# Performance work log

Measured on AMD Instinct MI355X. Metric: run time of the kernel, lower is better.

The kernel has to match this reference:

```python
import jax, jax.numpy as jnp
import numpy as np

B, L, H, NUM_LABELS = 4, 256, 768, 13


def setup_inputs() -> dict:
    key = jax.random.key(0)
    k1, k2, k3, k4, k5 = jax.random.split(key, 5)
    s1 = 1.0 / np.sqrt(2 * H)
    s2 = 1.0 / np.sqrt(H)
    return {
        "hidden_states": jax.random.normal(k1, (B, L, H), dtype=jnp.float32),
        "W1": jax.random.uniform(k2, (2 * H, H), jnp.float32, -s1, s1),
        "b1": jax.random.uniform(k3, (H,), jnp.float32, -s1, s1),
        "W2": jax.random.uniform(k4, (H, NUM_LABELS), jnp.float32, -s2, s2),
        "b2": jax.random.uniform(k5, (NUM_LABELS,), jnp.float32, -s2, s2),
    }


def reference(hidden_states, W1, b1, W2, b2):
    # Original: ffn(cat([x_start expand over dim2, x_end expand over dim1], -1))
    # Algebraically: Linear(2H->H) on the concat == proj(x_start) + proj(x_end)
    # broadcast over the L x L span grid, avoiding the (B,L,L,2H) tensor.
    H_ = hidden_states.shape[-1]
    xs_proj = jnp.einsum('bsh,hk->bsk', hidden_states, W1[:H_])   # start half
    xe_proj = jnp.einsum('bsh,hk->bsk', hidden_states, W1[H_:])   # end half
    h = xs_proj[:, :, None, :] + xe_proj[:, None, :, :] + b1      # (B,L,L,H)
    h = jax.nn.gelu(h, approximate=False)                         # torch GELU default = exact erf
    logits = jnp.einsum('bijk,kn->bijn', h, W2) + b2              # (B,L,L,num_labels)
    return logits
```

## Files before the change

### kernel.cpp

```cpp
#include <hip/hip_runtime.h>
#include <math.h>

#define H 768
#define L 256
#define NB 4
#define NL 13

typedef _Float16 h2 __attribute__((ext_vector_type(2)));
typedef _Float16 h4 __attribute__((ext_vector_type(4)));
typedef _Float16 half8 __attribute__((ext_vector_type(8)));
typedef float f32x4 __attribute__((ext_vector_type(4)));

__device__ inline h2 gelu_pk(h2 x) {
    const _Float16 kC = (_Float16)3.75f;
    h2 hi = {kC, kC}, lo = {(_Float16)-3.75f, (_Float16)-3.75f};
    h2 xc = __builtin_elementwise_min(__builtin_elementwise_max(x, lo), hi);
    h2 u = xc * xc;
    const _Float16 kE = (_Float16)0.125f;
    h2 ve = {kE, kE};
    h2 v = u * ve;
    const _Float16 d4v = (_Float16)0.0832840f,  d3v = (_Float16)-0.4335206f;
    const _Float16 d2v = (_Float16)0.8960128f,  d1v = (_Float16)-0.9876456f;
    const _Float16 d0v = (_Float16)0.7946463f;
    h2 d4 = {d4v, d4v}, d3 = {d3v, d3v}, d2 = {d2v, d2v}, d1 = {d1v, d1v}, d0 = {d0v, d0v};
    h2 p = v * (v * (v * (v * d4 + d3) + d2) + d1) + d0;
    h2 t = xc * p;
    const _Float16 kH = (_Float16)0.5f;
    h2 halfv = {kH, kH};
    h2 hx = x * halfv;
    return hx * t + hx;
}

__global__ __launch_bounds__(256) void gemm_fused(
    const float* __restrict__ X, const float* __restrict__ W1,
    const float* __restrict__ b1, const float* __restrict__ W2,
    _Float16* __restrict__ Pxs2, _Float16* __restrict__ Pxe,
    _Float16* __restrict__ Bfrag2)
{
    const int tid = threadIdx.x;

    if (blockIdx.y == 24) {
        int base = blockIdx.x * 768 + tid;
        #pragma unroll
        for (int r = 0; r < 3; ++r) {
            int idx = base + r * 256;
            int u = idx & 7;
            int lane = (idx >> 3) & 63;
            int kb = idx >> 9;
            int k = kb * 32 + ((lane >> 4) << 3) + u;
            int n = lane & 15;
            float v = (n < NL) ? W2[(size_t)k * NL + n] : 0.f;
            Bfrag2[idx] = (_Float16)v;
        }
        return;
    }

    __shared__ _Float16 As[64][72];
    __shared__ _Float16 Bs[64][72];
    const int w = tid >> 6, lane = tid & 63;
    const int ln = lane & 15, quad = lane >> 4;
    const int m0 = blockIdx.x * 64;
    const int n0g = blockIdx.y * 64;
    const bool isE = (n0g >= H);
    const float* Wb = W1 + (isE ? (size_t)H * H : 0);
    const int c0 = isE ? (n0g - H) : n0g;

    const int ar = tid >> 4;
    const int ac = (tid & 15) * 4;
    const int bc = (tid & 15) * 4;

    f32x4 acc[2][2] = {};
    for (int kr = 0; kr < H / 64; ++kr) {
        const int k0 = kr * 64;
        #pragma unroll
        for (int r = 0; r < 4; ++r) {
            int arow = r * 16 + ar;
            float4 f = *(const float4*)&X[(size_t)(m0 + arow) * H + k0 + ac];
            h4 o = { (_Float16)f.x, (_Float16)f.y, (_Float16)f.z, (_Float16)f.w };
            *(h4*)&As[arow][ac] = o;
        }
        #pragma unroll
        for (int r = 0; r < 2; ++r) {
            int kpl = r * 16 + (tid >> 4);
            const float* wr = &Wb[(size_t)(k0 + 2 * kpl) * H + c0 + bc];
            float4 fa = *(const float4*)wr;
            float4 fb = *(const float4*)(wr + H);
            h2 p0 = {(_Float16)fa.x, (_Float16)fb.x};
            h2 p1 = {(_Float16)fa.y, (_Float16)fb.y};
            h2 p2 = {(_Float16)fa.z, (_Float16)fb.z};
            h2 p3 = {(_Float16)fa.w, (_Float16)fb.w};
            *(h2*)&Bs[bc + 0][2 * kpl] = p0;
            *(h2*)&Bs[bc + 1][2 * kpl] = p1;
            *(h2*)&Bs[bc + 2][2 * kpl] = p2;
            *(h2*)&Bs[bc + 3][2 * kpl] = p3;
        }
        __syncthreads();
        #pragma unroll
        for (int sub = 0; sub < 2; ++sub) {
            const int ko = sub * 32 + quad * 8;
            half8 a0 = *(const half8*)&As[(w & 1) * 32 + ln][ko];
            half8 a1 = *(const half8*)&As[(w & 1) * 32 + 16 + ln][ko];
            half8 b0 = *(const half8*)&Bs[(w >> 1) * 32 + ln][ko];
            half8 b1f = *(const half8*)&Bs[(w >> 1) * 32 + 16 + ln][ko];
            acc[0][0] = __builtin_amdgcn_mfma_f32_16x16x32_f16(a0, b0, acc[0][0], 0, 0, 0);
            acc[0][1] = __builtin_amdgcn_mfma_f32_16x16x32_f16(a0, b1f, acc[0][1], 0, 0, 0);
            acc[1][0] = __builtin_amdgcn_mfma_f32_16x16x32_f16(a1, b0, acc[1][0], 0, 0, 0);
            acc[1][1] = __builtin_amdgcn_mfma_f32_16x16x32_f16(a1, b1f, acc[1][1], 0, 0, 0);
        }
        __syncthreads();
    }

    const int mb = m0 + (w & 1) * 32;
    const int nb = (w >> 1) * 32;
    if (!isE) {
        float bv[2] = { b1[n0g + nb + ln], b1[n0g + nb + 16 + ln] };
        #pragma unroll
        for (int mt = 0; mt < 2; ++mt)
            #pragma unroll
            for (int nt = 0; nt < 2; ++nt) {
                int n = n0g + nb + nt * 16 + ln;
                #pragma unroll
                for (int r = 0; r < 4; ++r) {
                    int m = mb + mt * 16 + quad * 4 + r;
                    Pxs2[(size_t)m * H + n] = (_Float16)(acc[mt][nt][r] + bv[nt]);
                }
            }
    } else {
        #pragma unroll
        for (int mt = 0; mt < 2; ++mt)
            #pragma unroll
            for (int nt = 0; nt < 2; ++nt) {
                int n = c0 + nb + nt * 16 + ln;
                #pragma unroll
                for (int r = 0; r < 4; ++r) {
                    int m = mb + mt * 16 + quad * 4 + r;
                    Pxe[(size_t)m * H + n] = (_Float16)acc[mt][nt][r];
                }
            }
    }
}

__global__ __launch_bounds__(256, 4) void span_mfma_kernel(
    const _Float16* __restrict__ Pxs2, const _Float16* __restrict__ Pxe,
    const _Float16* __restrict__ Bfrag2, const float* __restrict__ b2,
    float* __restrict__ out)
{
    __shared__ unsigned int xsf[4 * H / 2];
    const int ip = blockIdx.x >> 2;
    const int jq = blockIdx.x & 3;
    const int bi0 = ip * 4;
    const int b = bi0 >> 8;
    const int tid = threadIdx.x;

    const unsigned int* xsrc = (const unsigned int*)(Pxs2 + (size_t)bi0 * H);
    #pragma unroll
    for (int t = 0; t < 6; ++t) xsf[t * 256 + tid] = xsrc[t * 256 + tid];

    const int wave = tid >> 6;
    const int lane = tid & 63;
    const int n = lane & 15;
    const int quad = lane >> 4;
    const int j_load = jq * 64 + wave * 16 + n;

    const _Float16* xerow = Pxe + (size_t)(b * L + j_load) * H + quad * 8;
    const half8* bptr = (const half8*)(Bfrag2 + (size_t)lane * 8);

    f32x4 acc[4] = {};
    __syncthreads();

    for (int kb = 0; kb < H / 32; ++kb) {
        half8 bfrag = bptr[kb * 64];
        uint4 xev = *(const uint4*)(xerow + kb * 32);
        h2 xep[4] = { __builtin_bit_cast(h2, xev.x), __builtin_bit_cast(h2, xev.y),
                      __builtin_bit_cast(h2, xev.z), __builtin_bit_cast(h2, xev.w) };
        const int xo = kb * 16 + quad * 4;

        #pragma unroll
        for (int i01 = 0; i01 < 4; ++i01) {
            uint4 xsd = *(const uint4*)&xsf[i01 * (H / 2) + xo];
            h2 xsp[4] = { __builtin_bit_cast(h2, xsd.x), __builtin_bit_cast(h2, xsd.y),
                          __builtin_bit_cast(h2, xsd.z), __builtin_bit_cast(h2, xsd.w) };
            unsigned int pk[4];
            #pragma unroll
            for (int p = 0; p < 4; ++p) {
                h2 g = gelu_pk(xsp[p] + xep[p]);
                pk[p] = __builtin_bit_cast(unsigned int, g);
            }
            uint4 pk4 = {pk[0], pk[1], pk[2], pk[3]};
            half8 afrag = __builtin_bit_cast(half8, pk4);
            acc[i01] = __builtin_amdgcn_mfma_f32_16x16x32_f16(afrag, bfrag, acc[i01], 0, 0, 0);
        }
    }

    if (n < NL) {
        float b2v = b2[n];
        #pragma unroll
        for (int i01 = 0; i01 < 4; ++i01)
            #pragma unroll
            for (int r = 0; r < 4; ++r) {
                int j = jq * 64 + wave * 16 + quad * 4 + r;
                out[((size_t)(bi0 + i01) * L + j) * NL + n] = acc[i01][r] + b2v;
            }
    }
}

extern "C" void kernel_launch(void* const* d_in, const int* in_sizes, int n_in,
                              void* d_out, int out_size, void* d_ws, size_t ws_size,
                              hipStream_t stream)
{
    (void)in_sizes; (void)n_in; (void)out_size; (void)ws_size;
    const float* X  = (const float*)d_in[0];
    const float* W1 = (const float*)d_in[1];
    const float* b1 = (const float*)d_in[2];
    const float* W2 = (const float*)d_in[3];
    const float* b2 = (const float*)d_in[4];
    float* out = (float*)d_out;

    char* ws = (char*)d_ws;
    _Float16* Pxs2   = (_Float16*)ws;
    _Float16* Pxe    = Pxs2 + (size_t)NB * L * H;
    _Float16* Bfrag2 = Pxe + (size_t)NB * L * H;

    gemm_fused<<<dim3(16, 25), 256, 0, stream>>>(X, W1, b1, W2, Pxs2, Pxe, Bfrag2);
    span_mfma_kernel<<<NB * L, 256, 0, stream>>>(Pxs2, Pxe, Bfrag2, b2, out);
}
```

Baseline: 123.8 us.

## Merge projection GEMM and span kernel into one persistent ticket-scheduled kernel

Replaces the two launches with a single kernel of 1024 blocks. Blocks first take GEMM tiles through an atomic ticket counter and signal per-tile completion flags. Each block then spin-waits only on the flags for the start and end projection tiles it needs before running its span computation. W2 fragments are now rebuilt in LDS by every block rather than once in global memory. The goal is to remove the kernel boundary and overlap GEMM tail with span work, at the cost of a memset, atomics, spin-waiting, and more LDS per block, which may lower occupancy.

```diff
diff --git a/kernel.cpp b/kernel.cpp
--- a/kernel.cpp
+++ b/kernel.cpp
@@ -5,6 +5,9 @@
 #define L 256
 #define NB 4
 #define NL 13
+#define MT_TILES 16
+#define NT_TILES 24
+#define N_TICKETS (MT_TILES * NT_TILES)
 
 typedef _Float16 h2 __attribute__((ext_vector_type(2)));
 typedef _Float16 h4 __attribute__((ext_vector_type(4)));
@@ -31,145 +34,156 @@
     return hx * t + hx;
 }
 
-__global__ __launch_bounds__(256) void gemm_fused(
+__global__ __launch_bounds__(256, 3) void mono_kernel(
     const float* __restrict__ X, const float* __restrict__ W1,
     const float* __restrict__ b1, const float* __restrict__ W2,
+    const float* __restrict__ b2,
     _Float16* __restrict__ Pxs2, _Float16* __restrict__ Pxe,
-    _Float16* __restrict__ Bfrag2)
+    int* __restrict__ ctrl, float* __restrict__ out)
 {
-    const int tid = threadIdx.x;
-
-    if (blockIdx.y == 24) {
-        int base = blockIdx.x * 768 + tid;
-        #pragma unroll
-        for (int r = 0; r < 3; ++r) {
-            int idx = base + r * 256;
-            int u = idx & 7;
-            int lane = (idx >> 3) & 63;
-            int kb = idx >> 9;
-            int k = kb * 32 + ((lane >> 4) << 3) + u;
-            int n = lane & 15;
-            float v = (n < NL) ? W2[(size_t)k * NL + n] : 0.f;
-            Bfrag2[idx] = (_Float16)v;
-        }
-        return;
-    }
-
     __shared__ _Float16 As[64][72];
     __shared__ _Float16 Bs[64][72];
+    __shared__ _Float16 w2f[24 * 64 * 8];
+    __shared__ unsigned int xsf[4 * H / 2];
+    __shared__ int s_ticket;
+
+    const int tid = threadIdx.x;
     const int w = tid >> 6, lane = tid & 63;
     const int ln = lane & 15, quad = lane >> 4;
-    const int m0 = blockIdx.x * 64;
-    const int n0g = blockIdx.y * 64;
-    const bool isE = (n0g >= H);
-    const float* Wb = W1 + (isE ? (size_t)H * H : 0);
-    const int c0 = isE ? (n0g - H) : n0g;
-
-    const int ar = tid >> 4;
-    const int ac = (tid & 15) * 4;
-    const int bc = (tid & 15) * 4;
-
-    f32x4 acc[2][2] = {};
-    for (int kr = 0; kr < H / 64; ++kr) {
-        const int k0 = kr * 64;
-        #pragma unroll
-        for (int r = 0; r < 4; ++r) {
-            int arow = r * 16 + ar;
-            float4 f = *(const float4*)&X[(size_t)(m0 + arow) * H + k0 + ac];
-            h4 o = { (_Float16)f.x, (_Float16)f.y, (_Float16)f.z, (_Float16)f.w };
-            *(h4*)&As[arow][ac] = o;
+    int* ticket = ctrl;
+    int* flags  = ctrl + 1;
+
+    for (;;) {
+        __syncthreads();
+        if (tid == 0) s_ticket = atomicAdd(ticket, 1);
+        __syncthreads();
+        const int t = s_ticket;
+        if (t >= N_TICKETS) break;
+
+        const int mtile = t / NT_TILES;
+        const int ntile = t % NT_TILES;
+        const int m0 = mtile * 64;
+        const int n0g = ntile * 64;
+        const bool isE = (n0g >= H);
+        const float* Wb = W1 + (isE ? (size_t)H * H : 0);
+        const int c0 = isE ? (n0g - H) : n0g;
+
+        const int ar = tid >> 4;
+        const int ac = (tid & 15) * 4;
+        const int bc = (tid & 15) * 4;
+
+        f32x4 acc[2][2] = {};
+        for (int kr = 0; kr < H / 64; ++kr) {
+            const int k0 = kr * 64;
+            #pragma unroll
+            for (int r = 0; r < 4; ++r) {
+                int arow = r * 16 + ar;
+                float4 f = *(const float4*)&X[(size_t)(m0 + arow) * H + k0 + ac];
+                h4 o = { (_Float16)f.x, (_Float16)f.y, (_Float16)f.z, (_Float16)f.w };
+                *(h4*)&As[arow][ac] = o;
+            }
+            #pragma unroll
+            for (int r = 0; r < 2; ++r) {
+                int kpl = r * 16 + (tid >> 4);
+                const float* wr = &Wb[(size_t)(k0 + 2 * kpl) * H + c0 + bc];
+                float4 fa = *(const float4*)wr;
+                float4 fb = *(const float4*)(wr + H);
+                h2 p0 = {(_Float16)fa.x, (_Float16)fb.x};
+                h2 p1 = {(_Float16)fa.y, (_Float16)fb.y};
+                h2 p2 = {(_Float16)fa.z, (_Float16)fb.z};
+                h2 p3 = {(_Float16)fa.w, (_Float16)fb.w};
+                *(h2*)&Bs[bc + 0][2 * kpl] = p0;
+                *(h2*)&Bs[bc + 1][2 * kpl] = p1;
+                *(h2*)&Bs[bc + 2][2 * kpl] = p2;
+                *(h2*)&Bs[bc + 3][2 * kpl] = p3;
+            }
+            __syncthreads();
+            #pragma unroll
+            for (int sub = 0; sub < 2; ++sub) {
+                const int ko = sub * 32 + quad * 8;
+                half8 a0 = *(const half8*)&As[(w & 1) * 32 + ln][ko];
+                half8 a1 = *(const half8*)&As[(w & 1) * 32 + 16 + ln][ko];
+                half8 b0 = *(const half8*)&Bs[(w >> 1) * 32 + ln][ko];
+                half8 b1f = *(const half8*)&Bs[(w >> 1) * 32 + 16 + ln][ko];
+                acc[0][0] = __builtin_amdgcn_mfma_f32_16x16x32_f16(a0, b0, acc[0][0], 0, 0, 0);
+                acc[0][1] = __builtin_amdgcn_mfma_f32_16x16x32_f16(a0, b1f, acc[0][1], 0, 0, 0);
+                acc[1][0] = __builtin_amdgcn_mfma_f32_16x16x32_f16(a1, b0, acc[1][0], 0, 0, 0);
+                acc[1][1] = __builtin_amdgcn_mfma_f32_16x16x32_f16(a1, b1f, acc[1][1], 0, 0, 0);
+            }
+            __syncthreads();
         }
-        #pragma unroll
-        for (int r = 0; r < 2; ++r) {
-            int kpl = r * 16 + (tid >> 4);
-            const float* wr = &Wb[(size_t)(k0 + 2 * kpl) * H + c0 + bc];
-            float4 fa = *(const float4*)wr;
-            float4 fb = *(const float4*)(wr + H);
-            h2 p0 = {(_Float16)fa.x, (_Float16)fb.x};
-            h2 p1 = {(_Float16)fa.y, (_Float16)fb.y};
-            h2 p2 = {(_Float16)fa.z, (_Float16)fb.z};
-            h2 p3 = {(_Float16)fa.w, (_Float16)fb.w};
-            *(h2*)&Bs[bc + 0][2 * kpl] = p0;
-            *(h2*)&Bs[bc + 1][2 * kpl] = p1;
-            *(h2*)&Bs[bc + 2][2 * kpl] = p2;
-            *(h2*)&Bs[bc + 3][2 * kpl] = p3;
+
+        const int mb = m0 + (w & 1) * 32;
+        const int nb = (w >> 1) * 32;
+        if (!isE) {
+            float bv[2] = { b1[n0g + nb + ln], b1[n0g + nb + 16 + ln] };
+            #pragma unroll
+            for (int mt = 0; mt < 2; ++mt)
+                #pragma unroll
+                for (int nt = 0; nt < 2; ++nt) {
+                    int n = n0g + nb + nt * 16 + ln;
+                    #pragma unroll
+                    for (int r = 0; r < 4; ++r) {
+                        int m = mb + mt * 16 + quad * 4 + r;
+                        Pxs2[(size_t)m * H + n] = (_Float16)(acc[mt][nt][r] + bv[nt]);
+                    }
+                }
+        } else {
+            #pragma unroll
+            for (int mt = 0; mt < 2; ++mt)
+                #pragma unroll
+                for (int nt = 0; nt < 2; ++nt) {
+                    int n = c0 + nb + nt * 16 + ln;
+                    #pragma unroll
+                    for (int r = 0; r < 4; ++r) {
+                        int m = mb + mt * 16 + quad * 4 + r;
+                        Pxe[(size_t)m * H + n] = (_Float16)acc[mt][nt][r];
+                    }
+                }
         }
+        __threadfence();
         __syncthreads();
-        #pragma unroll
-        for (int sub = 0; sub < 2; ++sub) {
-            const int ko = sub * 32 + quad * 8;
-            half8 a0 = *(const half8*)&As[(w & 1) * 32 + ln][ko];
-            half8 a1 = *(const half8*)&As[(w & 1) * 32 + 16 + ln][ko];
-            half8 b0 = *(const half8*)&Bs[(w >> 1) * 32 + ln][ko];
-            half8 b1f = *(const half8*)&Bs[(w >> 1) * 32 + 16 + ln][ko];
-            acc[0][0] = __builtin_amdgcn_mfma_f32_16x16x32_f16(a0, b0, acc[0][0], 0, 0, 0);
-            acc[0][1] = __builtin_amdgcn_mfma_f32_16x16x32_f16(a0, b1f, acc[0][1], 0, 0, 0);
-            acc[1][0] = __builtin_amdgcn_mfma_f32_16x16x32_f16(a1, b0, acc[1][0], 0, 0, 0);
-            acc[1][1] = __builtin_amdgcn_mfma_f32_16x16x32_f16(a1, b1f, acc[1][1], 0, 0, 0);
-        }
-        __syncthreads();
-    }
-
-    const int mb = m0 + (w & 1) * 32;
-    const int nb = (w >> 1) * 32;
-    if (!isE) {
-        float bv[2] = { b1[n0g + nb + ln], b1[n0g + nb + 16 + ln] };
-        #pragma unroll
-        for (int mt = 0; mt < 2; ++mt)
-            #pragma unroll
-            for (int nt = 0; nt < 2; ++nt) {
-                int n = n0g + nb + nt * 16 + ln;
-                #pragma unroll
-                for (int r = 0; r < 4; ++r) {
-                    int m = mb + mt * 16 + quad * 4 + r;
-                    Pxs2[(size_t)m * H + n] = (_Float16)(acc[mt][nt][r] + bv[nt]);
-                }
-            }
-    } else {
-        #pragma unroll
-        for (int mt = 0; mt < 2; ++mt)
-            #pragma unroll
-            for (int nt = 0; nt < 2; ++nt) {
-                int n = c0 + nb + nt * 16 + ln;
-                #pragma unroll
-                for (int r = 0; r < 4; ++r) {
-                    int m = mb + mt * 16 + quad * 4 + r;
-                    Pxe[(size_t)m * H + n] = (_Float16)acc[mt][nt][r];
-                }
-            }
-    }
-}
-
-__global__ __launch_bounds__(256, 4) void span_mfma_kernel(
-    const _Float16* __restrict__ Pxs2, const _Float16* __restrict__ Pxe,
-    const _Float16* __restrict__ Bfrag2, const float* __restrict__ b2,
-    float* __restrict__ out)
-{
-    __shared__ unsigned int xsf[4 * H / 2];
+        if (tid == 0) atomicAdd(&flags[mtile * 2 + (isE ? 1 : 0)], 1);
+    }
+
+    #pragma unroll 4
+    for (int r = 0; r < 48; ++r) {
+        int idx = r * 256 + tid;
+        int u = idx & 7;
+        int l = (idx >> 3) & 63;
+        int kb = idx >> 9;
+        int k = kb * 32 + ((l >> 4) << 3) + u;
+        int n = l & 15;
+        float v = (n < NL) ? W2[(size_t)k * NL + n] : 0.f;
+        w2f[idx] = (_Float16)v;
+    }
+
     const int ip = blockIdx.x >> 2;
     const int jq = blockIdx.x & 3;
     const int bi0 = ip * 4;
     const int b = bi0 >> 8;
-    const int tid = threadIdx.x;
+    const int mt_i = ip >> 4;
+    const int mt_j = b * 4 + jq;
+
+    while (__hip_atomic_load(&flags[mt_i * 2 + 0], __ATOMIC_RELAXED, __HIP_MEMORY_SCOPE_AGENT) < 12 ||
+           __hip_atomic_load(&flags[mt_j * 2 + 1], __ATOMIC_RELAXED, __HIP_MEMORY_SCOPE_AGENT) < 12) {
+        __builtin_amdgcn_s_sleep(16);
+    }
+    __threadfence();
 
     const unsigned int* xsrc = (const unsigned int*)(Pxs2 + (size_t)bi0 * H);
     #pragma unroll
     for (int t = 0; t < 6; ++t) xsf[t * 256 + tid] = xsrc[t * 256 + tid];
 
-    const int wave = tid >> 6;
-    const int lane = tid & 63;
-    const int n = lane & 15;
-    const int quad = lane >> 4;
-    const int j_load = jq * 64 + wave * 16 + n;
-
+    const int n = ln;
+    const int j_load = jq * 64 + w * 16 + n;
     const _Float16* xerow = Pxe + (size_t)(b * L + j_load) * H + quad * 8;
-    const half8* bptr = (const half8*)(Bfrag2 + (size_t)lane * 8);
 
     f32x4 acc[4] = {};
     __syncthreads();
 
     for (int kb = 0; kb < H / 32; ++kb) {
-        half8 bfrag = bptr[kb * 64];
+        half8 bfrag = *(const half8*)&w2f[((size_t)kb * 64 + lane) * 8];
         uint4 xev = *(const uint4*)(xerow + kb * 32);
         h2 xep[4] = { __builtin_bit_cast(h2, xev.x), __builtin_bit_cast(h2, xev.y),
                       __builtin_bit_cast(h2, xev.z), __builtin_bit_cast(h2, xev.w) };
@@ -198,7 +212,7 @@
         for (int i01 = 0; i01 < 4; ++i01)
             #pragma unroll
             for (int r = 0; r < 4; ++r) {
-                int j = jq * 64 + wave * 16 + quad * 4 + r;
+                int j = jq * 64 + w * 16 + quad * 4 + r;
                 out[((size_t)(bi0 + i01) * L + j) * NL + n] = acc[i01][r] + b2v;
             }
     }
@@ -217,10 +231,10 @@
     float* out = (float*)d_out;
 
     char* ws = (char*)d_ws;
-    _Float16* Pxs2   = (_Float16*)ws;
-    _Float16* Pxe    = Pxs2 + (size_t)NB * L * H;
-    _Float16* Bfrag2 = Pxe + (size_t)NB * L * H;
-
-    gemm_fused<<<dim3(16, 25), 256, 0, stream>>>(X, W1, b1, W2, Pxs2, Pxe, Bfrag2);
-    span_mfma_kernel<<<NB * L, 256, 0, stream>>>(Pxs2, Pxe, Bfrag2, b2, out);
+    _Float16* Pxs2 = (_Float16*)ws;
+    _Float16* Pxe  = Pxs2 + (size_t)NB * L * H;
+    int* ctrl      = (int*)(Pxe + (size_t)NB * L * H);
+
+    hipMemsetAsync(ctrl, 0, 256, stream);
+    mono_kernel<<<1024, 256, 0, stream>>>(X, W1, b1, W2, b2, Pxs2, Pxe, ctrl, out);
 }
```

Result: slower. 320.4 us (+158.8%).
